# Optimization experiments

Measured on AMD Instinct MI355X. Metric: run time of the kernel, lower is better.

The kernel has to match this reference:

```python
import jax, jax.numpy as jnp
import numpy as np

G, T, E = 20000, 2, 4        # n_genes, n_tech, n_expansion
U = G * T                    # independent tiny-linear units
N_ETH = 4                    # ethnicity cardinality (interaction index stride)
DNN_DIMS = [20038, 5009, 1252, 313, 78, 2]  # shrinkage_factor=4, min=64, final=2


def setup_inputs() -> dict:
    key = jax.random.key(0)
    ks = jax.random.split(key, 24)
    B = 512
    inp = {
        "expression": jax.random.normal(ks[0], (B, T, G), jnp.float32),
        "clinical_categorical": jax.random.randint(ks[1], (B, 3), 0, 4),
        "clinical_non_categorical": jax.random.normal(ks[2], (B, 2, 10), jnp.float32),
        # ParallelBellowsLayers params
        "bw1": 0.05 * jax.random.normal(ks[3], (U, E), jnp.float32),
        "bb1": 0.05 * jax.random.normal(ks[4], (U, E), jnp.float32),
        "bw2": 0.05 * jax.random.normal(ks[5], (U, E), jnp.float32),
        "bb2": 0.05 * jax.random.normal(ks[6], (U,), jnp.float32),
        # ParallelGeneLayers params
        "gw": 0.05 * jax.random.normal(ks[7], (G, T), jnp.float32),
        "gb": 0.05 * jax.random.normal(ks[8], (G,), jnp.float32),
        # embeddings
        "race_emb": 0.05 * jax.random.normal(ks[9], (10, 8), jnp.float32),
        "eth_emb": 0.05 * jax.random.normal(ks[10], (4, 4), jnp.float32),
        "inter_emb": 0.05 * jax.random.normal(ks[11], (40, 8), jnp.float32),
        "prot_emb": 0.05 * jax.random.normal(ks[12], (20, 8), jnp.float32),
        # ClinicalMissingMask params (n_variables=10)
        "mask_w": 0.05 * jax.random.normal(ks[13], (10, 2), jnp.float32),
        "mask_b": 0.05 * jax.random.normal(ks[14], (10,), jnp.float32),
    }
    for i in range(5):
        din, dout = DNN_DIMS[i], DNN_DIMS[i + 1]
        inp[f"dnn_w{i}"] = (jax.random.normal(ks[15 + i], (din, dout), jnp.float32)
                             / jnp.sqrt(jnp.float32(din)))
        inp[f"dnn_b{i}"] = jnp.zeros((dout,), jnp.float32)
    return inp


def _forward(expression, clinical_categorical, clinical_non_categorical,
             bw1, bb1, bw2, bb2, gw, gb,
             race_emb, eth_emb, inter_emb, prot_emb, mask_w, mask_b,
             dnn_w0, dnn_b0, dnn_w1, dnn_b1, dnn_w2, dnn_b2,
             dnn_w3, dnn_b3, dnn_w4, dnn_b4):
    B = expression.shape[0]
    # --- CombinedGeneModel ---
    # bellows: per-unit 1->E->1 linear; units are tech-major (view(B,T,G))
    xf = expression.reshape(B, U)                              # [B, U]
    h = jax.nn.relu(xf[:, :, None] * bw1[None] + bb1[None])    # [B, U, E]
    s = jax.nn.relu(jnp.einsum('bue,ue->bu', h, bw2) + bb2)    # [B, U]
    # per-gene combine over tech
    s3 = s.reshape(B, T, G)
    expr = jax.nn.relu(jnp.einsum('btg,gt->bg', s3, gw) + gb)  # [B, G]
    # --- ClinicalModel ---
    cc = clinical_categorical
    race = race_emb[cc[:, 0]]
    eth = eth_emb[cc[:, 1]]
    inter = inter_emb[cc[:, 0] * N_ETH + cc[:, 1]]
    prot = prot_emb[cc[:, 2]]
    nc = jax.nn.relu(jnp.einsum('bcv,vc->bv', clinical_non_categorical, mask_w)
                     + mask_b)                                 # [B, 10]
    clin = jnp.concatenate([race, eth, inter, prot, nc], axis=1)
    # --- ConnectedLayers (shrinking MLP) ---
    x = jnp.concatenate([expr, clin], axis=1)                  # [B, 20038]
    for w, b in [(dnn_w0, dnn_b0), (dnn_w1, dnn_b1),
                 (dnn_w2, dnn_b2), (dnn_w3, dnn_b3)]:
        x = jax.nn.relu(x @ w + b)
    return x @ dnn_w4 + dnn_b4                                 # [B, 2]


def reference(expression, clinical_categorical, clinical_non_categorical,
              bw1, bb1, bw2, bb2, gw, gb,
              race_emb, eth_emb, inter_emb, prot_emb, mask_w, mask_b,
              dnn_w0, dnn_b0, dnn_w1, dnn_b1, dnn_w2, dnn_b2,
              dnn_w3, dnn_b3, dnn_w4, dnn_b4):
    return _forward(expression, clinical_categorical, clinical_non_categorical,
                    bw1, bb1, bw2, bb2, gw, gb,
                    race_emb, eth_emb, inter_emb, prot_emb, mask_w, mask_b,
                    dnn_w0, dnn_b0, dnn_w1, dnn_b1, dnn_w2, dnn_b2,
                    dnn_w3, dnn_b3, dnn_w4, dnn_b4)
```

## Files before the change

### kernel.cpp

```cpp
#include <hip/hip_runtime.h>
#include <hip/hip_bf16.h>

typedef __attribute__((ext_vector_type(8))) short bf16x8;
typedef __attribute__((ext_vector_type(4))) float f32x4;
typedef __attribute__((ext_vector_type(4))) int   i32x4;
typedef __attribute__((ext_vector_type(4))) unsigned short u16x4;
typedef unsigned short u16;

#define G_ 20000
#define B_ 512

__device__ __forceinline__ u16 f2bf(float x) {
  __hip_bfloat16 h = __float2bfloat16(x);
  return __builtin_bit_cast(u16, h);
}
__device__ __forceinline__ float bf2f(u16 u) {
  unsigned int v = ((unsigned int)u) << 16;
  return __builtin_bit_cast(float, v);
}

__global__ void k_gene(const float* __restrict__ expr,
                       const float* __restrict__ bw1, const float* __restrict__ bb1,
                       const float* __restrict__ bw2, const float* __restrict__ bb2,
                       const float* __restrict__ gw,  const float* __restrict__ gb,
                       u16* __restrict__ Xt) {
  int g = blockIdx.x * 256 + threadIdx.x;
  if (g >= G_) return;
  int b0 = blockIdx.y * 32;

  f32x4 w1a = ((const f32x4*)bw1)[g];
  f32x4 w1b = ((const f32x4*)bw1)[G_ + g];
  f32x4 b1a = ((const f32x4*)bb1)[g];
  f32x4 b1b = ((const f32x4*)bb1)[G_ + g];
  f32x4 w2a = ((const f32x4*)bw2)[g];
  f32x4 w2b = ((const f32x4*)bw2)[G_ + g];
  float bb2a = bb2[g], bb2b = bb2[G_ + g];
  float gw0 = gw[g * 2], gw1 = gw[g * 2 + 1];
  float gbg = gb[g];

  u16* outp = Xt + (size_t)(g >> 6) * 32768 + (g & 63);

  #pragma unroll 4
  for (int b = b0; b < b0 + 32; ++b) {
    float x0 = expr[(size_t)(b * 2) * G_ + g];
    float x1 = expr[(size_t)(b * 2 + 1) * G_ + g];
    float h0 = fmaxf(x0 * w1a.x + b1a.x, 0.f);
    float h1 = fmaxf(x0 * w1a.y + b1a.y, 0.f);
    float h2 = fmaxf(x0 * w1a.z + b1a.z, 0.f);
    float h3 = fmaxf(x0 * w1a.w + b1a.w, 0.f);
    float s0 = fmaxf(h0 * w2a.x + h1 * w2a.y + h2 * w2a.z + h3 * w2a.w + bb2a, 0.f);
    float g0 = fmaxf(x1 * w1b.x + b1b.x, 0.f);
    float g1 = fmaxf(x1 * w1b.y + b1b.y, 0.f);
    float g2 = fmaxf(x1 * w1b.z + b1b.z, 0.f);
    float g3 = fmaxf(x1 * w1b.w + b1b.w, 0.f);
    float s1 = fmaxf(g0 * w2b.x + g1 * w2b.y + g2 * w2b.z + g3 * w2b.w + bb2b, 0.f);
    float e = fmaxf(s0 * gw0 + s1 * gw1 + gbg, 0.f);
    outp[(size_t)b * 64] = f2bf(e);
  }
}

__global__ void k_clin(const int* __restrict__ cc, const float* __restrict__ cnc,
                       const float* __restrict__ race, const float* __restrict__ eth,
                       const float* __restrict__ inter, const float* __restrict__ prot,
                       const float* __restrict__ mw, const float* __restrict__ mb,
                       u16* __restrict__ Xt) {
  int b = threadIdx.x;
  int c0 = cc[b * 3], c1 = cc[b * 3 + 1], c2 = cc[b * 3 + 2];
  float nc[10];
  #pragma unroll
  for (int v = 0; v < 10; ++v)
    nc[v] = fmaxf(cnc[b * 20 + v] * mw[v * 2] + cnc[b * 20 + 10 + v] * mw[v * 2 + 1] + mb[v], 0.f);

  #pragma unroll
  for (int j = 0; j < 96; ++j) {
    float v;
    if (j < 8)       v = race[c0 * 8 + j];
    else if (j < 12) v = eth[c1 * 4 + (j - 8)];
    else if (j < 20) v = inter[(c0 * 4 + c1) * 8 + (j - 12)];
    else if (j < 28) v = prot[c2 * 8 + (j - 20)];
    else if (j < 38) v = nc[j - 28];
    else             v = 0.f;
    int k = 20000 + j;
    Xt[(size_t)(k >> 6) * 32768 + b * 64 + (k & 63)] = f2bf(v);
  }
}

__global__ __launch_bounds__(512, 2) void k_gemm(
    const u16* __restrict__ Xt, const float* __restrict__ W,
    float* __restrict__ part, int nSlabs, int Kvalid, int Nvalid, int Npad) {
  __shared__ __align__(16) u16 As[2][512 * 64];
  __shared__ __align__(16) u16 Bs[128 * 64];

  const int tid = threadIdx.x;
  const int nt = blockIdx.x, split = blockIdx.y, S = gridDim.y;
  const int n0 = nt * 128;
  const int s0 = (int)(((long)split * nSlabs) / S);
  const int s1 = (int)(((long)(split + 1) * nSlabs) / S);
  const int sLast = s1 - 1;

  const int lane = tid & 63, wave = tid >> 6;
  const int wr = wave >> 1, wc = wave & 1;
  const int l15 = lane & 15, l4 = lane >> 4;

  const int bn = tid & 127, bh = tid >> 7;
  const int nW = n0 + bn;
  const bool nok = nW < Nvalid;

  f32x4 acc[8][4];
  #pragma unroll
  for (int i = 0; i < 8; ++i)
    #pragma unroll
    for (int j = 0; j < 4; ++j)
      acc[i][j] = f32x4{0.f, 0.f, 0.f, 0.f};

  i32x4 areg[8];
  float wreg[16];

  auto ALOAD = [&](int s) {
    const i32x4* src = (const i32x4*)(Xt + (size_t)s * 32768);
    #pragma unroll
    for (int i = 0; i < 8; ++i) areg[i] = src[i * 512 + tid];
  };
  auto WLOAD = [&](int s) {
    int kb = s * 64 + bh * 16;
    #pragma unroll
    for (int j = 0; j < 16; ++j) {
      int k = kb + j;
      wreg[j] = (nok && k < Kvalid) ? W[(size_t)k * Nvalid + nW] : 0.f;
    }
  };
  auto ASTORE = [&](int buf) {
    #pragma unroll
    for (int i = 0; i < 8; ++i) {
      int lin = i * 512 + tid;
      int m = lin >> 3, cch = lin & 7;
      *(i32x4*)&As[buf][m * 64 + ((cch ^ (m & 7)) << 3)] = areg[i];
    }
  };
  auto BSTORE = [&]() {
    #pragma unroll
    for (int h = 0; h < 2; ++h) {
      i32x4 pk;
      #pragma unroll
      for (int q = 0; q < 4; ++q) {
        u16 lo = f2bf(wreg[h * 8 + q * 2]);
        u16 hi = f2bf(wreg[h * 8 + q * 2 + 1]);
        pk[q] = (int)(unsigned)lo | ((int)(unsigned)hi << 16);
      }
      int cch = bh * 2 + h;
      *(i32x4*)&Bs[bn * 64 + ((cch ^ (bn & 7)) << 3)] = pk;
    }
  };
  auto COMPUTE = [&](int buf) {
    #pragma unroll
    for (int kk = 0; kk < 2; ++kk) {
      bf16x8 bfr[4];
      #pragma unroll
      for (int nf = 0; nf < 4; ++nf) {
        int n = wc * 64 + nf * 16 + l15;
        int cch = kk * 4 + l4;
        bfr[nf] = *(const bf16x8*)&Bs[n * 64 + ((cch ^ (n & 7)) << 3)];
      }
      #pragma unroll
      for (int mf = 0; mf < 8; ++mf) {
        int m = wr * 128 + mf * 16 + l15;
        int cch = kk * 4 + l4;
        bf16x8 af = *(const bf16x8*)&As[buf][m * 64 + ((cch ^ (m & 7)) << 3)];
        #pragma unroll
        for (int nf = 0; nf < 4; ++nf)
          acc[mf][nf] = __builtin_amdgcn_mfma_f32_16x16x32_bf16(af, bfr[nf], acc[mf][nf], 0, 0, 0);
      }
    }
  };

  WLOAD(s0); ALOAD(s0);
  ASTORE(0); BSTORE();
  {
    int sn = (s0 + 1 > sLast) ? sLast : s0 + 1;
    ALOAD(sn); WLOAD(sn);
  }
  asm volatile("s_waitcnt lgkmcnt(0)" ::: "memory");
  __builtin_amdgcn_s_barrier();

  int c = 0;
  for (int s = s0; s < s1; ++s) {
    int sp = (s + 2 > sLast) ? sLast : s + 2;
    ASTORE(c ^ 1);
    ALOAD(sp);
    asm volatile("s_waitcnt lgkmcnt(0)" ::: "memory");
    __builtin_amdgcn_s_barrier();
    COMPUTE(c);
    __builtin_amdgcn_s_barrier();
    BSTORE();
    WLOAD(sp);
    c ^= 1;
  }

  float* outp = part + (size_t)split * B_ * Npad;
  #pragma unroll
  for (int mf = 0; mf < 8; ++mf)
    #pragma unroll
    for (int nf = 0; nf < 4; ++nf) {
      int col = n0 + wc * 64 + nf * 16 + l15;
      int rb = wr * 128 + mf * 16 + l4 * 4;
      #pragma unroll
      for (int r = 0; r < 4; ++r)
        outp[(size_t)(rb + r) * Npad + col] = acc[mf][nf][r];
    }
}

__global__ void k_reduce(const float* __restrict__ part, const float* __restrict__ bias,
                         u16* __restrict__ Ht, int S, int Npad, int Nout, int Nvalid) {
  int idx = blockIdx.x * 256 + threadIdx.x;
  int perRow = Nout >> 2;
  if (idx >= B_ * perRow) return;
  int b = idx / perRow;
  int n = (idx - b * perRow) * 4;
  float v[4] = {0.f, 0.f, 0.f, 0.f};
  for (int s = 0; s < S; ++s) {
    const f32x4 p = *(const f32x4*)&part[(size_t)s * B_ * Npad + (size_t)b * Npad + n];
    #pragma unroll
    for (int r = 0; r < 4; ++r) v[r] += p[r];
  }
  u16x4 o;
  #pragma unroll
  for (int r = 0; r < 4; ++r) {
    float bi = (n + r < Nvalid) ? bias[n + r] : 0.f;
    o[r] = f2bf(fmaxf(v[r] + bi, 0.f));
  }
  *(u16x4*)&Ht[(size_t)(n >> 6) * 32768 + b * 64 + (n & 63)] = o;
}

__global__ void k_tail(const u16* __restrict__ H3t,
                       const float* __restrict__ W3, const float* __restrict__ b3,
                       const float* __restrict__ W4, const float* __restrict__ b4,
                       float* __restrict__ out) {
  __shared__ float h3[320];
  __shared__ float h4[80];
  int b = blockIdx.x, tid = threadIdx.x;
  for (int i = tid; i < 313; i += 128)
    h3[i] = bf2f(H3t[(size_t)(i >> 6) * 32768 + b * 64 + (i & 63)]);
  __syncthreads();
  if (tid < 78) {
    float a = b3[tid];
    for (int k = 0; k < 313; ++k) a += h3[k] * W3[k * 78 + tid];
    h4[tid] = fmaxf(a, 0.f);
  }
  __syncthreads();
  if (tid < 2) {
    float a = b4[tid];
    for (int k = 0; k < 78; ++k) a += h4[k] * W4[k * 2 + tid];
    out[b * 2 + tid] = a;
  }
}

extern "C" void kernel_launch(void* const* d_in, const int* in_sizes, int n_in,
                              void* d_out, int out_size, void* d_ws, size_t ws_size,
                              hipStream_t stream) {
  const float* expr = (const float*)d_in[0];
  const int*   cc   = (const int*)d_in[1];
  const float* cnc  = (const float*)d_in[2];
  const float* bw1  = (const float*)d_in[3];
  const float* bb1  = (const float*)d_in[4];
  const float* bw2  = (const float*)d_in[5];
  const float* bb2  = (const float*)d_in[6];
  const float* gw   = (const float*)d_in[7];
  const float* gb   = (const float*)d_in[8];
  const float* race = (const float*)d_in[9];
  const float* eth  = (const float*)d_in[10];
  const float* inter= (const float*)d_in[11];
  const float* prot = (const float*)d_in[12];
  const float* mw   = (const float*)d_in[13];
  const float* mb   = (const float*)d_in[14];
  const float* w0 = (const float*)d_in[15]; const float* b0 = (const float*)d_in[16];
  const float* w1 = (const float*)d_in[17]; const float* b1 = (const float*)d_in[18];
  const float* w2 = (const float*)d_in[19]; const float* b2 = (const float*)d_in[20];
  const float* w3 = (const float*)d_in[21]; const float* b3 = (const float*)d_in[22];
  const float* w4 = (const float*)d_in[23]; const float* b4 = (const float*)d_in[24];

  u16* Xt  = (u16*)d_ws;
  u16* H1t = Xt  + (size_t)314 * 32768;
  u16* H2t = H1t + (size_t)80 * 32768;
  u16* H3t = H2t + (size_t)20 * 32768;
  float* part = (float*)(H3t + (size_t)5 * 32768);

  k_gene<<<dim3(79, 16), 256, 0, stream>>>(expr, bw1, bb1, bw2, bb2, gw, gb, Xt);
  k_clin<<<1, 512, 0, stream>>>(cc, cnc, race, eth, inter, prot, mw, mb, Xt);

  k_gemm<<<dim3(40, 6), 512, 0, stream>>>(Xt, w0, part, 314, 20038, 5009, 5120);
  k_reduce<<<2560, 256, 0, stream>>>(part, b0, H1t, 6, 5120, 5120, 5009);

  k_gemm<<<dim3(10, 12), 512, 0, stream>>>(H1t, w1, part, 80, 5009, 1252, 1280);
  k_reduce<<<640, 256, 0, stream>>>(part, b1, H2t, 12, 1280, 1280, 1252);

  k_gemm<<<dim3(3, 5), 512, 0, stream>>>(H2t, w2, part, 20, 1252, 313, 384);
  k_reduce<<<160, 256, 0, stream>>>(part, b2, H3t, 5, 384, 320, 313);

  k_tail<<<512, 128, 0, stream>>>(H3t, w3, b3, w4, b4, (float*)d_out);
}
```

Measured before the change: 323.5 us.

## Load GEMM A tiles directly into LDS with pre-swizzled global layout; fuse clinical kernel

The activation buffers are now written by producer kernels already in the XOR-swizzled layout the GEMM's shared-memory tile uses. This lets the GEMM copy A slabs straight from global memory into LDS with global_load_lds, dropping the register staging and the separate LDS store pass. The main loop is reordered so compute on one buffer overlaps the async load into the other, with explicit vmcnt waits and scheduling barriers. The clinical-feature kernel is folded into an extra column of blocks in the gene kernel, removing one launch. The risks are wrong vmcnt counts or ordering between the async loads and the barriers.

```diff
diff --git a/kernel.cpp b/kernel.cpp
--- a/kernel.cpp
+++ b/kernel.cpp
@@ -19,14 +19,53 @@
   return __builtin_bit_cast(float, v);
 }
 
+__device__ __forceinline__ void glds16(const void* g, void* l) {
+  __builtin_amdgcn_global_load_lds(
+      (const __attribute__((address_space(1))) void*)g,
+      (__attribute__((address_space(3))) void*)l, 16, 0, 0);
+}
+
+__device__ __forceinline__ int swz(int b, int kk) {
+  return b * 64 + ((((kk >> 3) & 7) ^ (b & 7)) << 3) + (kk & 7);
+}
+
 __global__ void k_gene(const float* __restrict__ expr,
                        const float* __restrict__ bw1, const float* __restrict__ bb1,
                        const float* __restrict__ bw2, const float* __restrict__ bb2,
                        const float* __restrict__ gw,  const float* __restrict__ gb,
+                       const int* __restrict__ cc, const float* __restrict__ cnc,
+                       const float* __restrict__ race, const float* __restrict__ eth,
+                       const float* __restrict__ inter, const float* __restrict__ prot,
+                       const float* __restrict__ mw, const float* __restrict__ mb,
                        u16* __restrict__ Xt) {
+  int b0 = blockIdx.y * 32;
+
+  if (blockIdx.x == 79) {
+    int b = b0 + (threadIdx.x >> 3);
+    int j0 = (threadIdx.x & 7) * 12;
+    int c0 = cc[b * 3], c1 = cc[b * 3 + 1], c2 = cc[b * 3 + 2];
+    float nc[10];
+    #pragma unroll
+    for (int v = 0; v < 10; ++v)
+      nc[v] = fmaxf(cnc[b * 20 + v] * mw[v * 2] + cnc[b * 20 + 10 + v] * mw[v * 2 + 1] + mb[v], 0.f);
+    #pragma unroll
+    for (int jj = 0; jj < 12; ++jj) {
+      int j = j0 + jj;
+      float v;
+      if (j < 8)       v = race[c0 * 8 + j];
+      else if (j < 12) v = eth[c1 * 4 + (j - 8)];
+      else if (j < 20) v = inter[(c0 * 4 + c1) * 8 + (j - 12)];
+      else if (j < 28) v = prot[c2 * 8 + (j - 20)];
+      else if (j < 38) v = nc[j - 28];
+      else             v = 0.f;
+      int k = 20000 + j;
+      Xt[(size_t)(k >> 6) * 32768 + swz(b, k & 63)] = f2bf(v);
+    }
+    return;
+  }
+
   int g = blockIdx.x * 256 + threadIdx.x;
   if (g >= G_) return;
-  int b0 = blockIdx.y * 32;
 
   f32x4 w1a = ((const f32x4*)bw1)[g];
   f32x4 w1b = ((const f32x4*)bw1)[G_ + g];
@@ -38,7 +77,8 @@
   float gw0 = gw[g * 2], gw1 = gw[g * 2 + 1];
   float gbg = gb[g];
 
-  u16* outp = Xt + (size_t)(g >> 6) * 32768 + (g & 63);
+  u16* slab = Xt + (size_t)(g >> 6) * 32768;
+  int kk = g & 63, ch = (kk >> 3) & 7, klo = kk & 7;
 
   #pragma unroll 4
   for (int b = b0; b < b0 + 32; ++b) {
@@ -55,33 +95,7 @@
     float g3 = fmaxf(x1 * w1b.w + b1b.w, 0.f);
     float s1 = fmaxf(g0 * w2b.x + g1 * w2b.y + g2 * w2b.z + g3 * w2b.w + bb2b, 0.f);
     float e = fmaxf(s0 * gw0 + s1 * gw1 + gbg, 0.f);
-    outp[(size_t)b * 64] = f2bf(e);
-  }
-}
-
-__global__ void k_clin(const int* __restrict__ cc, const float* __restrict__ cnc,
-                       const float* __restrict__ race, const float* __restrict__ eth,
-                       const float* __restrict__ inter, const float* __restrict__ prot,
-                       const float* __restrict__ mw, const float* __restrict__ mb,
-                       u16* __restrict__ Xt) {
-  int b = threadIdx.x;
-  int c0 = cc[b * 3], c1 = cc[b * 3 + 1], c2 = cc[b * 3 + 2];
-  float nc[10];
-  #pragma unroll
-  for (int v = 0; v < 10; ++v)
-    nc[v] = fmaxf(cnc[b * 20 + v] * mw[v * 2] + cnc[b * 20 + 10 + v] * mw[v * 2 + 1] + mb[v], 0.f);
-
-  #pragma unroll
-  for (int j = 0; j < 96; ++j) {
-    float v;
-    if (j < 8)       v = race[c0 * 8 + j];
-    else if (j < 12) v = eth[c1 * 4 + (j - 8)];
-    else if (j < 20) v = inter[(c0 * 4 + c1) * 8 + (j - 12)];
-    else if (j < 28) v = prot[c2 * 8 + (j - 20)];
-    else if (j < 38) v = nc[j - 28];
-    else             v = 0.f;
-    int k = 20000 + j;
-    Xt[(size_t)(k >> 6) * 32768 + b * 64 + (k & 63)] = f2bf(v);
+    slab[b * 64 + ((ch ^ (b & 7)) << 3) + klo] = f2bf(e);
   }
 }
 
@@ -98,10 +112,9 @@
   const int s1 = (int)(((long)(split + 1) * nSlabs) / S);
   const int sLast = s1 - 1;
 
-  const int lane = tid & 63, wave = tid >> 6;
-  const int wr = wave >> 1, wc = wave & 1;
+  const int lane = tid & 63, wv = tid >> 6;
+  const int wr = wv >> 1, wc = wv & 1;
   const int l15 = lane & 15, l4 = lane >> 4;
-
   const int bn = tid & 127, bh = tid >> 7;
   const int nW = n0 + bn;
   const bool nok = nW < Nvalid;
@@ -113,13 +126,16 @@
     for (int j = 0; j < 4; ++j)
       acc[i][j] = f32x4{0.f, 0.f, 0.f, 0.f};
 
-  i32x4 areg[8];
   float wreg[16];
 
-  auto ALOAD = [&](int s) {
-    const i32x4* src = (const i32x4*)(Xt + (size_t)s * 32768);
-    #pragma unroll
-    for (int i = 0; i < 8; ++i) areg[i] = src[i * 512 + tid];
+  auto GLDS = [&](int s, int buf) {
+    const char* sb = (const char*)(Xt + (size_t)s * 32768);
+    char* lb = (char*)&As[buf][0];
+    #pragma unroll
+    for (int j = 0; j < 8; ++j) {
+      int q = wv * 8 + j;
+      glds16(sb + q * 1024 + lane * 16, lb + q * 1024);
+    }
   };
   auto WLOAD = [&](int s) {
     int kb = s * 64 + bh * 16;
@@ -127,14 +143,6 @@
     for (int j = 0; j < 16; ++j) {
       int k = kb + j;
       wreg[j] = (nok && k < Kvalid) ? W[(size_t)k * Nvalid + nW] : 0.f;
-    }
-  };
-  auto ASTORE = [&](int buf) {
-    #pragma unroll
-    for (int i = 0; i < 8; ++i) {
-      int lin = i * 512 + tid;
-      int m = lin >> 3, cch = lin & 7;
-      *(i32x4*)&As[buf][m * 64 + ((cch ^ (m & 7)) << 3)] = areg[i];
     }
   };
   auto BSTORE = [&]() {
@@ -173,26 +181,28 @@
     }
   };
 
-  WLOAD(s0); ALOAD(s0);
-  ASTORE(0); BSTORE();
-  {
-    int sn = (s0 + 1 > sLast) ? sLast : s0 + 1;
-    ALOAD(sn); WLOAD(sn);
-  }
+  GLDS(s0, 0); WLOAD(s0);
+  asm volatile("s_waitcnt vmcnt(0)" ::: "memory");
+  BSTORE();
+  int sp1 = (s0 + 1 > sLast) ? sLast : s0 + 1;
+  GLDS(sp1, 1); WLOAD(sp1);
   asm volatile("s_waitcnt lgkmcnt(0)" ::: "memory");
   __builtin_amdgcn_s_barrier();
+  __builtin_amdgcn_sched_barrier(0);
 
   int c = 0;
   for (int s = s0; s < s1; ++s) {
+    COMPUTE(c);
+    __builtin_amdgcn_s_barrier();
+    __builtin_amdgcn_sched_barrier(0);
     int sp = (s + 2 > sLast) ? sLast : s + 2;
-    ASTORE(c ^ 1);
-    ALOAD(sp);
+    GLDS(sp, c);
+    asm volatile("s_waitcnt vmcnt(8)" ::: "memory");
+    BSTORE();
+    WLOAD(sp);
     asm volatile("s_waitcnt lgkmcnt(0)" ::: "memory");
     __builtin_amdgcn_s_barrier();
-    COMPUTE(c);
-    __builtin_amdgcn_s_barrier();
-    BSTORE();
-    WLOAD(sp);
+    __builtin_amdgcn_sched_barrier(0);
     c ^= 1;
   }
 
@@ -228,7 +238,7 @@
     float bi = (n + r < Nvalid) ? bias[n + r] : 0.f;
     o[r] = f2bf(fmaxf(v[r] + bi, 0.f));
   }
-  *(u16x4*)&Ht[(size_t)(n >> 6) * 32768 + b * 64 + (n & 63)] = o;
+  *(u16x4*)&Ht[(size_t)(n >> 6) * 32768 + swz(b, n & 63)] = o;
 }
 
 __global__ void k_tail(const u16* __restrict__ H3t,
@@ -239,10 +249,11 @@
   __shared__ float h4[80];
   int b = blockIdx.x, tid = threadIdx.x;
   for (int i = tid; i < 313; i += 128)
-    h3[i] = bf2f(H3t[(size_t)(i >> 6) * 32768 + b * 64 + (i & 63)]);
+    h3[i] = bf2f(H3t[(size_t)(i >> 6) * 32768 + swz(b, i & 63)]);
   __syncthreads();
   if (tid < 78) {
     float a = b3[tid];
+    #pragma unroll 4
     for (int k = 0; k < 313; ++k) a += h3[k] * W3[k * 78 + tid];
     h4[tid] = fmaxf(a, 0.f);
   }
@@ -284,8 +295,8 @@
   u16* H3t = H2t + (size_t)20 * 32768;
   float* part = (float*)(H3t + (size_t)5 * 32768);
 
-  k_gene<<<dim3(79, 16), 256, 0, stream>>>(expr, bw1, bb1, bw2, bb2, gw, gb, Xt);
-  k_clin<<<1, 512, 0, stream>>>(cc, cnc, race, eth, inter, prot, mw, mb, Xt);
+  k_gene<<<dim3(80, 16), 256, 0, stream>>>(expr, bw1, bb1, bw2, bb2, gw, gb,
+                                           cc, cnc, race, eth, inter, prot, mw, mb, Xt);
 
   k_gemm<<<dim3(40, 6), 512, 0, stream>>>(Xt, w0, part, 314, 20038, 5009, 5120);
   k_reduce<<<2560, 256, 0, stream>>>(part, b0, H1t, 6, 5120, 5120, 5009);
```

Result: slower. 336.1 us (+3.9%).
